# Performance work log

Measured on AMD Instinct MI355X. Metric: run time of the kernel, lower is better.

The kernel has to match this reference:

```python
import jax, jax.numpy as jnp
import numpy as np

D_MODEL = 1024
N_HEADS = 16
D_HEAD = D_MODEL // N_HEADS


def setup_inputs() -> dict:
    key = jax.random.key(0)
    ks = jax.random.split(key, 9)
    B, S = 2, 2048
    s = 0.02
    return {
        "x": jax.random.normal(ks[0], (B, S, D_MODEL), dtype=jnp.float32),
        "Wq": jax.random.normal(ks[1], (D_MODEL, D_MODEL), dtype=jnp.float32) * s,
        "bq": jnp.zeros((D_MODEL,), dtype=jnp.float32),
        "Wk": jax.random.normal(ks[2], (D_MODEL, D_MODEL), dtype=jnp.float32) * s,
        "bk": jnp.zeros((D_MODEL,), dtype=jnp.float32),
        "Wv": jax.random.normal(ks[3], (D_MODEL, D_MODEL), dtype=jnp.float32) * s,
        "bv": jnp.zeros((D_MODEL,), dtype=jnp.float32),
        "Wo": jax.random.normal(ks[4], (D_MODEL, D_MODEL), dtype=jnp.float32) * s,
        "bo": jnp.zeros((D_MODEL,), dtype=jnp.float32),
    }


def reference(x, Wq, bq, Wk, bk, Wv, bv, Wo, bo):
    B, S, _ = x.shape
    # projections -> [B, H, S, Dh]
    def split_heads(t):
        return t.reshape(B, S, N_HEADS, D_HEAD).transpose(0, 2, 1, 3)
    Q = split_heads(x @ Wq + bq)
    K = split_heads(x @ Wk + bk)
    V = split_heads(x @ Wv + bv)
    scores = jnp.einsum('bhqd,bhkd->bhqk', Q, K)  # [B,H,S,S]
    mask = jnp.tril(jnp.ones((S, S), dtype=bool))
    # NB: original masks BEFORE scaling (mask fill -1e9 then /sqrt(d_head))
    scores = jnp.where(mask[None, None], scores, jnp.float32(-1e9))
    scores = scores / jnp.sqrt(jnp.float32(D_HEAD))
    attn = jax.nn.softmax(scores, axis=-1)
    ctx = jnp.einsum('bhqk,bhkd->bhqd', attn, V)
    ctx = ctx.transpose(0, 2, 1, 3).reshape(B, S, D_MODEL)
    return ctx @ Wo + bo
```

## Files before the change

### kernel.cpp

```cpp
#include <hip/hip_runtime.h>

typedef __bf16 bf16;
typedef __bf16 bf16x8 __attribute__((ext_vector_type(8)));
typedef __bf16 bf16x4 __attribute__((ext_vector_type(4)));
typedef float  f32x4  __attribute__((ext_vector_type(4)));

#define D_MODEL 1024
#define S_LEN   2048
#define NHEAD   16
#define DHEAD   64
#define BATCH   2
#define MROWS   (BATCH * S_LEN)

#define QSCALE 0.18033688011112042f

__device__ __forceinline__ void gld_lds16(const void* g, void* lds_base) {
    __builtin_amdgcn_global_load_lds(
        (const __attribute__((address_space(1))) void*)g,
        (__attribute__((address_space(3))) void*)lds_base, 16, 0, 0);
}

__global__ void prep_kernel(const float* __restrict__ x,
                            const float* __restrict__ W0, const float* __restrict__ W1,
                            const float* __restrict__ W2, const float* __restrict__ W3,
                            bf16* __restrict__ xb, bf16* __restrict__ Wt) {
    int tx = threadIdx.x, ty = threadIdx.y;
    if (blockIdx.z == 4) {
        int tid = ty * 32 + tx;
        size_t base = ((size_t)blockIdx.y * 32 + blockIdx.x) * 4096;
#pragma unroll
        for (int j = 0; j < 4; j++) {
            size_t i = base + (size_t)(j * 256 + tid) * 4;
            f32x4 v = *(const f32x4*)(x + i);
            bf16x4 o;
            o[0] = (bf16)v[0]; o[1] = (bf16)v[1]; o[2] = (bf16)v[2]; o[3] = (bf16)v[3];
            *(bf16x4*)(xb + i) = o;
        }
        return;
    }
    __shared__ float tile[32][33];
    const float* W = (blockIdx.z == 0) ? W0 : (blockIdx.z == 1) ? W1
                   : (blockIdx.z == 2) ? W2 : W3;
    int n0 = blockIdx.x * 32, k0 = blockIdx.y * 32;
#pragma unroll
    for (int j = 0; j < 4; j++)
        tile[ty + 8 * j][tx] = W[(size_t)(k0 + ty + 8 * j) * D_MODEL + n0 + tx];
    __syncthreads();
    bf16* out = Wt + (size_t)blockIdx.z * D_MODEL * D_MODEL;
#pragma unroll
    for (int j = 0; j < 4; j++)
        out[(size_t)(n0 + ty + 8 * j) * D_MODEL + k0 + tx] = (bf16)tile[tx][ty + 8 * j];
}

__global__ __launch_bounds__(256, 3) void gemm0_kernel(
    const bf16* __restrict__ A, const bf16* __restrict__ Bt,
    const float* __restrict__ b0, const float* __restrict__ b1, const float* __restrict__ b2,
    bf16* __restrict__ Qo, bf16* __restrict__ Ko, bf16* __restrict__ Vto) {
    __shared__ bf16 sA[2][128 * 64];
    __shared__ bf16 sB[2][64 * 64];
    const int t = threadIdx.x;
    const int wave = t >> 6, lane = t & 63;
    const int quad = lane >> 4, m16 = lane & 15;
    const int wrow = wave * 32;
    const int row0 = blockIdx.y * 128, col0 = blockIdx.x * 64;
    constexpr int NK = D_MODEL / 64;

    f32x4 acc[2][4];
#pragma unroll
    for (int i = 0; i < 2; i++)
#pragma unroll
        for (int j = 0; j < 4; j++) acc[i][j] = (f32x4){0.f, 0.f, 0.f, 0.f};

    auto stage = [&](int kk, int buf) {
#pragma unroll
        for (int i = 0; i < 4; i++) {
            int cb = i * 256 + wave * 64;
            int c  = cb + lane;
            int r  = c >> 3, sl = c & 7;
            int gk = sl ^ (r & 7);
            gld_lds16(A + (size_t)(row0 + r) * D_MODEL + kk * 64 + gk * 8,
                      (char*)&sA[buf][0] + cb * 16);
        }
#pragma unroll
        for (int i = 0; i < 2; i++) {
            int cb = i * 256 + wave * 64;
            int c  = cb + lane;
            int r  = c >> 3, sl = c & 7;
            int gk = sl ^ (r & 7);
            gld_lds16(Bt + (size_t)(col0 + r) * D_MODEL + kk * 64 + gk * 8,
                      (char*)&sB[buf][0] + cb * 16);
        }
    };

    stage(0, 0);

    const int s7 = m16 & 7;
    for (int ks = 0; ks < NK; ++ks) {
        asm volatile("s_waitcnt vmcnt(0)\n\ts_barrier" ::: "memory");
        if (ks + 1 < NK) stage(ks + 1, (ks + 1) & 1);

        const int cur = ks & 1;
        bf16x8 af[2][2], bfr[4][2];
#pragma unroll
        for (int mi = 0; mi < 2; mi++)
#pragma unroll
            for (int kst = 0; kst < 2; kst++) {
                int g = kst * 4 + quad;
                af[mi][kst] = *(const bf16x8*)
                    &sA[cur][(wrow + mi * 16 + m16) * 64 + (g ^ s7) * 8];
            }
#pragma unroll
        for (int ni = 0; ni < 4; ni++)
#pragma unroll
            for (int kst = 0; kst < 2; kst++) {
                int g = kst * 4 + quad;
                bfr[ni][kst] = *(const bf16x8*)
                    &sB[cur][(ni * 16 + m16) * 64 + (g ^ s7) * 8];
            }
#pragma unroll
        for (int kst = 0; kst < 2; kst++)
#pragma unroll
            for (int mi = 0; mi < 2; mi++)
#pragma unroll
                for (int ni = 0; ni < 4; ni++)
                    acc[mi][ni] = __builtin_amdgcn_mfma_f32_16x16x32_bf16(
                        af[mi][kst], bfr[ni][kst], acc[mi][ni], 0, 0, 0);
    }

    int sel = col0 >> 10;
    const float* bias_arr = (sel == 0) ? b0 : (sel == 1) ? b1 : b2;
#pragma unroll
    for (int mi = 0; mi < 2; mi++) {
        int s0g = row0 + wrow + mi * 16 + quad * 4;
        int b = s0g >> 11, ss0 = s0g & 2047;
#pragma unroll
        for (int ni = 0; ni < 4; ni++) {
            int col = col0 + ni * 16 + m16;
            int cn = col & 1023;
            int h = cn >> 6, d = cn & 63;
            float bias = bias_arr[cn];
            if (sel < 2) {
                bf16* dst = (sel == 0) ? Qo : Ko;
                float scl = (sel == 0) ? QSCALE : 1.0f;
                size_t base = (((size_t)b * NHEAD + h) * S_LEN);
#pragma unroll
                for (int r = 0; r < 4; r++)
                    dst[(base + ss0 + r) * DHEAD + d] = (bf16)((acc[mi][ni][r] + bias) * scl);
            } else {
                bf16x4 pk;
#pragma unroll
                for (int r = 0; r < 4; r++) pk[r] = (bf16)(acc[mi][ni][r] + bias);
                *(bf16x4*)(Vto + (((size_t)b * NHEAD + h) * DHEAD + d) * S_LEN + ss0) = pk;
            }
        }
    }
}

__global__ __launch_bounds__(512, 4) void gemm1_kernel(
    const bf16* __restrict__ A, const bf16* __restrict__ Bt,
    const float* __restrict__ bias, float* __restrict__ Co) {
    __shared__ bf16 sA[3][2][128 * 32];
    __shared__ bf16 sB[3][2][64 * 32];
    const int t = threadIdx.x;
    const int wave = t >> 6, lane = t & 63;
    const int quad = lane >> 4, m16 = lane & 15;
    const int grp = wave >> 2, w4 = wave & 3;
    const int wrow = w4 * 32;
    const int row0 = blockIdx.y * 128, col0 = blockIdx.x * 64;
    const int kbase = grp * 512;
    constexpr int NK = 16;

    f32x4 acc[2][4];
#pragma unroll
    for (int i = 0; i < 2; i++)
#pragma unroll
        for (int j = 0; j < 4; j++) acc[i][j] = (f32x4){0.f, 0.f, 0.f, 0.f};

    auto stage = [&](int kk, int buf) {
#pragma unroll
        for (int i = 0; i < 2; i++) {
            int cb = i * 256 + w4 * 64;
            int c  = cb + lane;
            int r  = c >> 2, kg = c & 3;
            int gk = kg ^ ((r >> 1) & 3);
            gld_lds16(A + (size_t)(row0 + r) * D_MODEL + kbase + kk * 32 + gk * 8,
                      (char*)&sA[buf][grp][0] + cb * 16);
        }
        {
            int cb = w4 * 64;
            int c  = cb + lane;
            int r  = c >> 2, kg = c & 3;
            int gk = kg ^ ((r >> 1) & 3);
            gld_lds16(Bt + (size_t)(col0 + r) * D_MODEL + kbase + kk * 32 + gk * 8,
                      (char*)&sB[buf][grp][0] + cb * 16);
        }
    };

    stage(0, 0);
    stage(1, 1);

    const int sx = (m16 >> 1) & 3;
    for (int ks = 0; ks < NK; ++ks) {
        if (ks + 1 < NK)
            asm volatile("s_waitcnt vmcnt(3)\n\ts_barrier" ::: "memory");
        else
            asm volatile("s_waitcnt vmcnt(0)\n\ts_barrier" ::: "memory");
        if (ks + 2 < NK) stage(ks + 2, (ks + 2) % 3);

        const int cur = ks % 3;
        const int gg = (quad ^ sx) * 8;
        bf16x8 af[2], bfr[4];
#pragma unroll
        for (int mi = 0; mi < 2; mi++)
            af[mi] = *(const bf16x8*)&sA[cur][grp][(wrow + mi * 16 + m16) * 32 + gg];
#pragma unroll
        for (int ni = 0; ni < 4; ni++)
            bfr[ni] = *(const bf16x8*)&sB[cur][grp][(ni * 16 + m16) * 32 + gg];
#pragma unroll
        for (int mi = 0; mi < 2; mi++)
#pragma unroll
            for (int ni = 0; ni < 4; ni++)
                acc[mi][ni] = __builtin_amdgcn_mfma_f32_16x16x32_bf16(
                    af[mi], bfr[ni], acc[mi][ni], 0, 0, 0);
    }

    __syncthreads();
    float* scr = (float*)&sA[0][0][0];
    if (grp == 1) {
#pragma unroll
        for (int mi = 0; mi < 2; mi++)
#pragma unroll
            for (int ni = 0; ni < 4; ni++)
#pragma unroll
                for (int r = 0; r < 4; r++)
                    scr[(wrow + mi * 16 + quad * 4 + r) * 66 + ni * 16 + m16] =
                        acc[mi][ni][r];
    }
    __syncthreads();
    if (grp == 0) {
#pragma unroll
        for (int mi = 0; mi < 2; mi++)
#pragma unroll
            for (int ni = 0; ni < 4; ni++) {
                int col = col0 + ni * 16 + m16;
                float bb = bias[col];
#pragma unroll
                for (int r = 0; r < 4; r++) {
                    int row = wrow + mi * 16 + quad * 4 + r;
                    Co[(size_t)(row0 + row) * D_MODEL + col] =
                        acc[mi][ni][r] + scr[row * 66 + ni * 16 + m16] + bb;
                }
            }
    }
}

__global__ __launch_bounds__(256, 4) void attn_kernel(
    const bf16* __restrict__ Q, const bf16* __restrict__ K,
    const bf16* __restrict__ Vt, bf16* __restrict__ ctx) {
    __shared__ bf16 Kt_s[2][64 * 64];
    __shared__ bf16 Vt_s[2][64 * 64];

    const int t = threadIdx.x, wave = t >> 6, lane = t & 63;
    const int quad = lane >> 4, m16 = lane & 15;
    const int bh = blockIdx.x;
    const int qt = 31 - blockIdx.y;
    const int nt = qt + 1;
    const size_t base = (size_t)bh * S_LEN * DHEAD;

    bf16x8 aq[2];
#pragma unroll
    for (int kst = 0; kst < 2; kst++)
        aq[kst] = *(const bf16x8*)(Q + base
            + (size_t)(qt * 64 + wave * 16 + m16) * DHEAD + kst * 32 + quad * 8);

    f32x4 o[4];
#pragma unroll
    for (int di = 0; di < 4; di++) o[di] = (f32x4){0.f, 0.f, 0.f, 0.f};
    float l_acc = 0.f;

    auto stage = [&](int j, int buf) {
#pragma unroll
        for (int i = 0; i < 2; i++) {
            int cb = i * 256 + wave * 64;
            int c  = cb + lane;
            int pos = c >> 3, g = c & 7;
            int gk = g ^ (pos & 7);
            gld_lds16(K  + base + (size_t)(j * 64 + pos) * DHEAD + gk * 8,
                      (char*)&Kt_s[buf][0] + cb * 16);
            gld_lds16(Vt + base + (size_t)pos * S_LEN + j * 64 + gk * 8,
                      (char*)&Vt_s[buf][0] + cb * 16);
        }
    };

    stage(0, 0);

    for (int j = 0; j < nt; ++j) {
        asm volatile("s_waitcnt vmcnt(0)\n\ts_barrier" ::: "memory");
        if (j + 1 < nt) stage(j + 1, (j + 1) & 1);

        const int cur = j & 1;
        const int kt0 = j * 64;

        f32x4 sc[4];
#pragma unroll
        for (int ni = 0; ni < 4; ni++) sc[ni] = (f32x4){0.f, 0.f, 0.f, 0.f};
        __builtin_amdgcn_s_setprio(1);
#pragma unroll
        for (int ni = 0; ni < 4; ni++) {
            int pos = ni * 16 + m16;
#pragma unroll
            for (int kst = 0; kst < 2; kst++) {
                int gg = (kst * 4 + quad) ^ (pos & 7);
                bf16x8 kf = *(const bf16x8*)&Kt_s[cur][pos * 64 + gg * 8];
                sc[ni] = __builtin_amdgcn_mfma_f32_16x16x32_bf16(
                    kf, aq[kst], sc[ni], 0, 0, 0);
            }
        }
        __builtin_amdgcn_s_setprio(0);

        if (j == qt) {
            int qg = qt * 64 + wave * 16 + m16;
#pragma unroll
            for (int ni = 0; ni < 4; ni++)
#pragma unroll
                for (int r = 0; r < 4; r++) {
                    int kp = kt0 + ni * 16 + quad * 4 + r;
                    if (kp > qg) sc[ni][r] = -1e9f;
                }
        }

        unsigned int pd[4][2];
        {
            float ls0 = 0.f, ls1 = 0.f;
#pragma unroll
            for (int ni = 0; ni < 4; ni++) {
                float p0 = __builtin_amdgcn_exp2f(sc[ni][0]);
                float p1 = __builtin_amdgcn_exp2f(sc[ni][1]);
                float p2 = __builtin_amdgcn_exp2f(sc[ni][2]);
                float p3 = __builtin_amdgcn_exp2f(sc[ni][3]);
                union { bf16x4 h; unsigned int u[2]; } cv;
                cv.h[0] = (bf16)p0; cv.h[1] = (bf16)p1;
                cv.h[2] = (bf16)p2; cv.h[3] = (bf16)p3;
                pd[ni][0] = cv.u[0];
                pd[ni][1] = cv.u[1];
                ls0 += p0 + p1;
                ls1 += p2 + p3;
            }
            l_acc += ls0 + ls1;
        }

#pragma unroll
        for (int kst = 0; kst < 2; kst++) {
            unsigned int x0 = pd[2 * kst][0],     y0 = pd[2 * kst][1];
            unsigned int x1 = pd[2 * kst + 1][0], y1 = pd[2 * kst + 1][1];
            asm("v_permlane32_swap_b32 %0, %1" : "+v"(x0), "+v"(x1));
            asm("v_permlane32_swap_b32 %0, %1" : "+v"(y0), "+v"(y1));
            asm("v_permlane16_swap_b32 %0, %1" : "+v"(x0), "+v"(x1));
            asm("v_permlane16_swap_b32 %0, %1" : "+v"(y0), "+v"(y1));
            union { unsigned int u[4]; bf16x8 v; } pk;
            pk.u[0] = x0; pk.u[1] = y0; pk.u[2] = x1; pk.u[3] = y1;
            bf16x8 ap = pk.v;
            __builtin_amdgcn_s_setprio(1);
#pragma unroll
            for (int di = 0; di < 4; di++) {
                int d = di * 16 + m16;
                int gg = (kst * 4 + quad) ^ (d & 7);
                bf16x8 vf = *(const bf16x8*)&Vt_s[cur][d * 64 + gg * 8];
                o[di] = __builtin_amdgcn_mfma_f32_16x16x32_bf16(
                    vf, ap, o[di], 0, 0, 0);
            }
            __builtin_amdgcn_s_setprio(0);
        }
    }

    int b = bh >> 4, h = bh & 15;
    float l = l_acc;
    l += __shfl_xor(l, 16);
    l += __shfl_xor(l, 32);
    float rl = 1.0f / l;
    int s = qt * 64 + wave * 16 + m16;
#pragma unroll
    for (int di = 0; di < 4; di++) {
        bf16x4 pk;
#pragma unroll
        for (int r = 0; r < 4; r++) pk[r] = (bf16)(o[di][r] * rl);
        *(bf16x4*)(ctx + ((size_t)b * S_LEN + s) * D_MODEL
                   + h * DHEAD + di * 16 + quad * 4) = pk;
    }
}

extern "C" void kernel_launch(void* const* d_in, const int* in_sizes, int n_in,
                              void* d_out, int out_size, void* d_ws, size_t ws_size,
                              hipStream_t stream) {
    const float* x  = (const float*)d_in[0];
    const float* Wq = (const float*)d_in[1];
    const float* bq = (const float*)d_in[2];
    const float* Wk = (const float*)d_in[3];
    const float* bk = (const float*)d_in[4];
    const float* Wv = (const float*)d_in[5];
    const float* bv = (const float*)d_in[6];
    const float* Wo = (const float*)d_in[7];
    const float* bo = (const float*)d_in[8];
    float* out = (float*)d_out;

    char* ws = (char*)d_ws;
    const size_t MB = 1u << 20;
    bf16* xb  = (bf16*)(ws + 0);
    bf16* Wt  = (bf16*)(ws + 8  * MB);
    bf16* Qb  = (bf16*)(ws + 16 * MB);
    bf16* Kb  = (bf16*)(ws + 24 * MB);
    bf16* Vtb = (bf16*)(ws + 32 * MB);
    bf16* ctx = (bf16*)(ws + 0);

    prep_kernel<<<dim3(32, 32, 5), dim3(32, 8), 0, stream>>>(x, Wq, Wk, Wv, Wo, xb, Wt);
    gemm0_kernel<<<dim3(48, 32), 256, 0, stream>>>(xb, Wt, bq, bk, bv,
                                                   Qb, Kb, Vtb);
    attn_kernel<<<dim3(32, 32), 256, 0, stream>>>(Qb, Kb, Vtb, ctx);
    gemm1_kernel<<<dim3(16, 32), 512, 0, stream>>>(ctx, Wt + 3 * 1024 * 1024,
                                                   bo, out);
}
```

Baseline: 177.4 us.

## Retile QKV GEMM to 128x128 with triple-buffered K=32 stages; swizzle output GEMM blocks

The QKV projection GEMM moves from 128x64 tiles with a double-buffered K=64 pipeline to 128x128 tiles, where each wave computes a 64x64 sub-tile from a triple-buffered K=32 pipeline. The wait now uses a partial vmcnt, so one stage can stay in flight while the next is computed. Larger tiles raise MFMA work per LDS load and halve the grid, at the cost of more accumulator registers and possibly lower occupancy. The output-projection GEMM now uses a 1D grid with a remapped block order, grouping row tiles for better L2 locality.

```diff
diff --git a/kernel.cpp b/kernel.cpp
--- a/kernel.cpp
+++ b/kernel.cpp
@@ -56,86 +56,79 @@
     const bf16* __restrict__ A, const bf16* __restrict__ Bt,
     const float* __restrict__ b0, const float* __restrict__ b1, const float* __restrict__ b2,
     bf16* __restrict__ Qo, bf16* __restrict__ Ko, bf16* __restrict__ Vto) {
-    __shared__ bf16 sA[2][128 * 64];
-    __shared__ bf16 sB[2][64 * 64];
+    __shared__ bf16 sA[3][128 * 32];
+    __shared__ bf16 sB[3][128 * 32];
     const int t = threadIdx.x;
     const int wave = t >> 6, lane = t & 63;
     const int quad = lane >> 4, m16 = lane & 15;
-    const int wrow = wave * 32;
-    const int row0 = blockIdx.y * 128, col0 = blockIdx.x * 64;
-    constexpr int NK = D_MODEL / 64;
-
-    f32x4 acc[2][4];
-#pragma unroll
-    for (int i = 0; i < 2; i++)
+    const int wrow = (wave >> 1) * 64, wcol = (wave & 1) * 64;
+    const int row0 = blockIdx.y * 128, col0 = blockIdx.x * 128;
+    constexpr int NK = D_MODEL / 32;
+
+    f32x4 acc[4][4];
+#pragma unroll
+    for (int i = 0; i < 4; i++)
 #pragma unroll
         for (int j = 0; j < 4; j++) acc[i][j] = (f32x4){0.f, 0.f, 0.f, 0.f};
 
     auto stage = [&](int kk, int buf) {
-#pragma unroll
-        for (int i = 0; i < 4; i++) {
-            int cb = i * 256 + wave * 64;
-            int c  = cb + lane;
-            int r  = c >> 3, sl = c & 7;
-            int gk = sl ^ (r & 7);
-            gld_lds16(A + (size_t)(row0 + r) * D_MODEL + kk * 64 + gk * 8,
-                      (char*)&sA[buf][0] + cb * 16);
-        }
 #pragma unroll
         for (int i = 0; i < 2; i++) {
             int cb = i * 256 + wave * 64;
             int c  = cb + lane;
-            int r  = c >> 3, sl = c & 7;
-            int gk = sl ^ (r & 7);
-            gld_lds16(Bt + (size_t)(col0 + r) * D_MODEL + kk * 64 + gk * 8,
+            int r  = c >> 2, kg = c & 3;
+            int gk = kg ^ ((r >> 1) & 3);
+            gld_lds16(A + (size_t)(row0 + r) * D_MODEL + kk * 32 + gk * 8,
+                      (char*)&sA[buf][0] + cb * 16);
+        }
+#pragma unroll
+        for (int i = 0; i < 2; i++) {
+            int cb = i * 256 + wave * 64;
+            int c  = cb + lane;
+            int r  = c >> 2, kg = c & 3;
+            int gk = kg ^ ((r >> 1) & 3);
+            gld_lds16(Bt + (size_t)(col0 + r) * D_MODEL + kk * 32 + gk * 8,
                       (char*)&sB[buf][0] + cb * 16);
         }
     };
 
     stage(0, 0);
-
-    const int s7 = m16 & 7;
+    stage(1, 1);
+
+    const int sx = (m16 >> 1) & 3;
     for (int ks = 0; ks < NK; ++ks) {
-        asm volatile("s_waitcnt vmcnt(0)\n\ts_barrier" ::: "memory");
-        if (ks + 1 < NK) stage(ks + 1, (ks + 1) & 1);
-
-        const int cur = ks & 1;
-        bf16x8 af[2][2], bfr[4][2];
-#pragma unroll
-        for (int mi = 0; mi < 2; mi++)
-#pragma unroll
-            for (int kst = 0; kst < 2; kst++) {
-                int g = kst * 4 + quad;
-                af[mi][kst] = *(const bf16x8*)
-                    &sA[cur][(wrow + mi * 16 + m16) * 64 + (g ^ s7) * 8];
-            }
+        if (ks + 1 < NK)
+            asm volatile("s_waitcnt vmcnt(4)\n\ts_barrier" ::: "memory");
+        else
+            asm volatile("s_waitcnt vmcnt(0)\n\ts_barrier" ::: "memory");
+        if (ks + 2 < NK) stage(ks + 2, (ks + 2) % 3);
+
+        const int cur = ks % 3;
+        const int gg = (quad ^ sx) * 8;
+        bf16x8 af[4], bfr[4];
+#pragma unroll
+        for (int mi = 0; mi < 4; mi++)
+            af[mi] = *(const bf16x8*)&sA[cur][(wrow + mi * 16 + m16) * 32 + gg];
 #pragma unroll
         for (int ni = 0; ni < 4; ni++)
-#pragma unroll
-            for (int kst = 0; kst < 2; kst++) {
-                int g = kst * 4 + quad;
-                bfr[ni][kst] = *(const bf16x8*)
-                    &sB[cur][(ni * 16 + m16) * 64 + (g ^ s7) * 8];
-            }
-#pragma unroll
-        for (int kst = 0; kst < 2; kst++)
-#pragma unroll
-            for (int mi = 0; mi < 2; mi++)
-#pragma unroll
-                for (int ni = 0; ni < 4; ni++)
-                    acc[mi][ni] = __builtin_amdgcn_mfma_f32_16x16x32_bf16(
-                        af[mi][kst], bfr[ni][kst], acc[mi][ni], 0, 0, 0);
+            bfr[ni] = *(const bf16x8*)&sB[cur][(wcol + ni * 16 + m16) * 32 + gg];
+#pragma unroll
+        for (int mi = 0; mi < 4; mi++)
+#pragma unroll
+            for (int ni = 0; ni < 4; ni++)
+                acc[mi][ni] = __builtin_amdgcn_mfma_f32_16x16x32_bf16(
+                    af[mi], bfr[ni], acc[mi][ni], 0, 0, 0);
     }
 
     int sel = col0 >> 10;
     const float* bias_arr = (sel == 0) ? b0 : (sel == 1) ? b1 : b2;
 #pragma unroll
-    for (int mi = 0; mi < 2; mi++) {
+    for (int mi = 0; mi < 4; mi++) {
         int s0g = row0 + wrow + mi * 16 + quad * 4;
         int b = s0g >> 11, ss0 = s0g & 2047;
 #pragma unroll
         for (int ni = 0; ni < 4; ni++) {
-            int col = col0 + ni * 16 + m16;
+            int col = col0 + wcol + ni * 16 + m16;
             int cn = col & 1023;
             int h = cn >> 6, d = cn & 63;
             float bias = bias_arr[cn];
@@ -166,7 +159,10 @@
     const int quad = lane >> 4, m16 = lane & 15;
     const int grp = wave >> 2, w4 = wave & 3;
     const int wrow = w4 * 32;
-    const int row0 = blockIdx.y * 128, col0 = blockIdx.x * 64;
+    const int p  = blockIdx.x;
+    const int xb = (p >> 3) & 15;
+    const int yb = (p & 7) + 8 * (p >> 7);
+    const int row0 = yb * 128, col0 = xb * 64;
     const int kbase = grp * 512;
     constexpr int NK = 16;
 
@@ -412,10 +408,11 @@
     bf16* Vtb = (bf16*)(ws + 32 * MB);
     bf16* ctx = (bf16*)(ws + 0);
 
-    prep_kernel<<<dim3(32, 32, 5), dim3(32, 8), 0, stream>>>(x, Wq, Wk, Wv, Wo, xb, Wt);
-    gemm0_kernel<<<dim3(48, 32), 256, 0, stream>>>(xb, Wt, bq, bk, bv,
+    prep_kernel<<<dim3(32, 32, 5), dim3(32, 8), 0, stream>>>(x, Wq, Wk, Wv, Wo,
+                                                             xb, Wt);
+    gemm0_kernel<<<dim3(24, 32), 256, 0, stream>>>(xb, Wt, bq, bk, bv,
                                                    Qb, Kb, Vtb);
     attn_kernel<<<dim3(32, 32), 256, 0, stream>>>(Qb, Kb, Vtb, ctx);
-    gemm1_kernel<<<dim3(16, 32), 512, 0, stream>>>(ctx, Wt + 3 * 1024 * 1024,
-                                                   bo, out);
-}
+    gemm1_kernel<<<dim3(512), 512, 0, stream>>>(ctx, Wt + 3 * 1024 * 1024,
+                                                bo, out);
+}
```

After: 175.9 us. About the same (-0.9%).

## Retile QKV GEMM to 256x256 blocks with staged pipeline and swizzled grids

Applied to the files above, without the earlier changes.

The QKV projection GEMM moves from 128x64 tiles with 4 waves to 256x256 tiles with 8 waves. Each wave computes a 128x64 sub-tile split into four quadrant phases, and loads of the next K tiles are interleaved between those phases. Wave priority is raised around the MFMA bursts. Both GEMMs now launch a 1D grid remapped for L2/XCD locality. This raises arithmetic intensity and cuts redundant global traffic, at the cost of only 192 blocks (under one wave on 256 CUs), much larger accumulator register pressure, and 128KB of LDS per block.

```diff
diff --git a/kernel.cpp b/kernel.cpp
--- a/kernel.cpp
+++ b/kernel.cpp
@@ -52,90 +52,121 @@
         out[(size_t)(n0 + ty + 8 * j) * D_MODEL + k0 + tx] = (bf16)tile[tx][ty + 8 * j];
 }
 
-__global__ __launch_bounds__(256, 3) void gemm0_kernel(
+__global__ __launch_bounds__(512, 2) void gemm0_kernel(
     const bf16* __restrict__ A, const bf16* __restrict__ Bt,
     const float* __restrict__ b0, const float* __restrict__ b1, const float* __restrict__ b2,
     bf16* __restrict__ Qo, bf16* __restrict__ Ko, bf16* __restrict__ Vto) {
-    __shared__ bf16 sA[2][128 * 64];
-    __shared__ bf16 sB[2][64 * 64];
+    __shared__ bf16 sA[2][2][128 * 64];
+    __shared__ bf16 sB[2][2][128 * 64];
     const int t = threadIdx.x;
     const int wave = t >> 6, lane = t & 63;
     const int quad = lane >> 4, m16 = lane & 15;
-    const int wrow = wave * 32;
-    const int row0 = blockIdx.y * 128, col0 = blockIdx.x * 64;
-    constexpr int NK = D_MODEL / 64;
-
-    f32x4 acc[2][4];
-#pragma unroll
-    for (int i = 0; i < 2; i++)
+    const int wm = wave >> 2, wn = wave & 3;
+    const int s7 = m16 & 7;
+    const int p   = blockIdx.x;
+    const int r8  = p & 7;
+    const int idx = p >> 3;
+    const int xl  = idx % 6, yl = idx / 6;
+    const int xb2 = (r8 & 1) * 6 + xl;
+    const int yb2 = (r8 >> 1) * 4 + yl;
+    const int row0 = yb2 * 256, col0 = xb2 * 256;
+    constexpr int NKT = D_MODEL / 64;
+
+    f32x4 acc[8][4];
+#pragma unroll
+    for (int i = 0; i < 8; i++)
 #pragma unroll
         for (int j = 0; j < 4; j++) acc[i][j] = (f32x4){0.f, 0.f, 0.f, 0.f};
 
-    auto stage = [&](int kk, int buf) {
-#pragma unroll
-        for (int i = 0; i < 4; i++) {
-            int cb = i * 256 + wave * 64;
+    auto stageA = [&](int T, int slot, int h) {
+#pragma unroll
+        for (int i = 0; i < 2; i++) {
+            int cb = i * 512 + wave * 64;
             int c  = cb + lane;
             int r  = c >> 3, sl = c & 7;
             int gk = sl ^ (r & 7);
-            gld_lds16(A + (size_t)(row0 + r) * D_MODEL + kk * 64 + gk * 8,
-                      (char*)&sA[buf][0] + cb * 16);
-        }
+            gld_lds16(A + (size_t)(row0 + h * 128 + r) * D_MODEL + T * 64 + gk * 8,
+                      (char*)&sA[slot][h][0] + cb * 16);
+        }
+    };
+    auto stageB = [&](int T, int slot, int h) {
 #pragma unroll
         for (int i = 0; i < 2; i++) {
-            int cb = i * 256 + wave * 64;
+            int cb = i * 512 + wave * 64;
             int c  = cb + lane;
             int r  = c >> 3, sl = c & 7;
             int gk = sl ^ (r & 7);
-            gld_lds16(Bt + (size_t)(col0 + r) * D_MODEL + kk * 64 + gk * 8,
-                      (char*)&sB[buf][0] + cb * 16);
+            gld_lds16(Bt + (size_t)(col0 + h * 128 + r) * D_MODEL + T * 64 + gk * 8,
+                      (char*)&sB[slot][h][0] + cb * 16);
         }
     };
 
-    stage(0, 0);
-
-    const int s7 = m16 & 7;
-    for (int ks = 0; ks < NK; ++ks) {
-        asm volatile("s_waitcnt vmcnt(0)\n\ts_barrier" ::: "memory");
-        if (ks + 1 < NK) stage(ks + 1, (ks + 1) & 1);
-
-        const int cur = ks & 1;
-        bf16x8 af[2][2], bfr[4][2];
-#pragma unroll
-        for (int mi = 0; mi < 2; mi++)
-#pragma unroll
-            for (int kst = 0; kst < 2; kst++) {
-                int g = kst * 4 + quad;
-                af[mi][kst] = *(const bf16x8*)
-                    &sA[cur][(wrow + mi * 16 + m16) * 64 + (g ^ s7) * 8];
-            }
-#pragma unroll
-        for (int ni = 0; ni < 4; ni++)
-#pragma unroll
-            for (int kst = 0; kst < 2; kst++) {
-                int g = kst * 4 + quad;
-                bfr[ni][kst] = *(const bf16x8*)
-                    &sB[cur][(ni * 16 + m16) * 64 + (g ^ s7) * 8];
-            }
-#pragma unroll
-        for (int kst = 0; kst < 2; kst++)
-#pragma unroll
-            for (int mi = 0; mi < 2; mi++)
-#pragma unroll
-                for (int ni = 0; ni < 4; ni++)
-                    acc[mi][ni] = __builtin_amdgcn_mfma_f32_16x16x32_bf16(
-                        af[mi][kst], bfr[ni][kst], acc[mi][ni], 0, 0, 0);
+    stageA(0, 0, 0); stageB(0, 0, 0);
+    stageA(0, 0, 1); stageB(0, 0, 1);
+    stageA(1, 1, 0); stageB(1, 1, 0);
+    asm volatile("s_waitcnt vmcnt(4)" ::: "memory");
+    asm volatile("s_barrier" ::: "memory");
+
+    for (int T = 0; T < NKT; ++T) {
+        const int s = T & 1;
+#pragma unroll
+        for (int q = 0; q < 4; ++q) {
+            const int qa = q >> 1, qb = q & 1;
+            const bf16* Ah = &sA[s][qa][0];
+            const bf16* Bh = &sB[s][qb][0];
+            bf16x8 af[4][2], bfr[2][2];
+#pragma unroll
+            for (int mi = 0; mi < 4; mi++)
+#pragma unroll
+                for (int kst = 0; kst < 2; kst++)
+                    af[mi][kst] = *(const bf16x8*)
+                        &Ah[(wm * 64 + mi * 16 + m16) * 64
+                            + (((kst * 4 + quad) ^ s7) * 8)];
+#pragma unroll
+            for (int ni = 0; ni < 2; ni++)
+#pragma unroll
+                for (int kst = 0; kst < 2; kst++)
+                    bfr[ni][kst] = *(const bf16x8*)
+                        &Bh[(wn * 32 + ni * 16 + m16) * 64
+                            + (((kst * 4 + quad) ^ s7) * 8)];
+            if (q == 0)      { if (T + 1 < NKT) stageA(T + 1, s ^ 1, 1); }
+            else if (q == 1) { if (T + 1 < NKT) stageB(T + 1, s ^ 1, 1); }
+            else if (q == 2) { if (T + 2 < NKT) stageA(T + 2, s, 0); }
+            else             { if (T + 2 < NKT) stageB(T + 2, s, 0); }
+            asm volatile("s_barrier" ::: "memory");
+            __builtin_amdgcn_s_setprio(1);
+#pragma unroll
+            for (int kst = 0; kst < 2; kst++)
+#pragma unroll
+                for (int mi = 0; mi < 4; mi++)
+#pragma unroll
+                    for (int ni = 0; ni < 2; ni++)
+                        acc[qa * 4 + mi][qb * 2 + ni] =
+                            __builtin_amdgcn_mfma_f32_16x16x32_bf16(
+                                af[mi][kst], bfr[ni][kst],
+                                acc[qa * 4 + mi][qb * 2 + ni], 0, 0, 0);
+            __builtin_amdgcn_s_setprio(0);
+            if (q == 3) {
+                if (T < NKT - 2)
+                    asm volatile("s_waitcnt vmcnt(4)" ::: "memory");
+                else if (T == NKT - 2)
+                    asm volatile("s_waitcnt vmcnt(0)" ::: "memory");
+            }
+            asm volatile("s_barrier" ::: "memory");
+        }
     }
 
     int sel = col0 >> 10;
     const float* bias_arr = (sel == 0) ? b0 : (sel == 1) ? b1 : b2;
 #pragma unroll
-    for (int mi = 0; mi < 2; mi++) {
-        int s0g = row0 + wrow + mi * 16 + quad * 4;
+    for (int a = 0; a < 8; a++) {
+        int ha = a >> 2, mi = a & 3;
+        int s0g = row0 + ha * 128 + wm * 64 + mi * 16 + quad * 4;
         int b = s0g >> 11, ss0 = s0g & 2047;
 #pragma unroll
-        for (int ni = 0; ni < 4; ni++) {
-            int col = col0 + ni * 16 + m16;
+        for (int c2 = 0; c2 < 4; c2++) {
+            int hb = c2 >> 1, ni = c2 & 1;
+            int col = col0 + hb * 128 + wn * 32 + ni * 16 + m16;
             int cn = col & 1023;
             int h = cn >> 6, d = cn & 63;
             float bias = bias_arr[cn];
@@ -145,11 +176,12 @@
                 size_t base = (((size_t)b * NHEAD + h) * S_LEN);
 #pragma unroll
                 for (int r = 0; r < 4; r++)
-                    dst[(base + ss0 + r) * DHEAD + d] = (bf16)((acc[mi][ni][r] + bias) * scl);
+                    dst[(base + ss0 + r) * DHEAD + d] =
+                        (bf16)((acc[a][c2][r] + bias) * scl);
             } else {
                 bf16x4 pk;
 #pragma unroll
-                for (int r = 0; r < 4; r++) pk[r] = (bf16)(acc[mi][ni][r] + bias);
+                for (int r = 0; r < 4; r++) pk[r] = (bf16)(acc[a][c2][r] + bias);
                 *(bf16x4*)(Vto + (((size_t)b * NHEAD + h) * DHEAD + d) * S_LEN + ss0) = pk;
             }
         }
@@ -166,7 +198,10 @@
     const int quad = lane >> 4, m16 = lane & 15;
     const int grp = wave >> 2, w4 = wave & 3;
     const int wrow = w4 * 32;
-    const int row0 = blockIdx.y * 128, col0 = blockIdx.x * 64;
+    const int p  = blockIdx.x;
+    const int xb = (p >> 3) & 15;
+    const int yb = (p & 7) + 8 * (p >> 7);
+    const int row0 = yb * 128, col0 = xb * 64;
     const int kbase = grp * 512;
     constexpr int NK = 16;
 
@@ -412,10 +447,11 @@
     bf16* Vtb = (bf16*)(ws + 32 * MB);
     bf16* ctx = (bf16*)(ws + 0);
 
-    prep_kernel<<<dim3(32, 32, 5), dim3(32, 8), 0, stream>>>(x, Wq, Wk, Wv, Wo, xb, Wt);
-    gemm0_kernel<<<dim3(48, 32), 256, 0, stream>>>(xb, Wt, bq, bk, bv,
-                                                   Qb, Kb, Vtb);
+    prep_kernel<<<dim3(32, 32, 5), dim3(32, 8), 0, stream>>>(x, Wq, Wk, Wv, Wo,
+                                                             xb, Wt);
+    gemm0_kernel<<<dim3(192), 512, 0, stream>>>(xb, Wt, bq, bk, bv,
+                                                Qb, Kb, Vtb);
     attn_kernel<<<dim3(32, 32), 256, 0, stream>>>(Qb, Kb, Vtb, ctx);
-    gemm1_kernel<<<dim3(16, 32), 512, 0, stream>>>(ctx, Wt + 3 * 1024 * 1024,
-                                                   bo, out);
-}
+    gemm1_kernel<<<dim3(512), 512, 0, stream>>>(ctx, Wt + 3 * 1024 * 1024,
+                                                bo, out);
+}
```

New measurement: 188.0 us. +5.9%, slower.
